# Kernel optimization log

Hardware: AMD Instinct MI355X
Metric: run time of the kernel (lower is better)

## Reference

```python
import jax, jax.numpy as jnp
import numpy as np

B, N, DX, E, H, HD, KH, FF = 8, 8192, 2, 128, 8, 16, 32, 128
G1, G2, PMAX = 32, 32, 32


def _ln(x, g, b):
    mu = jnp.mean(x, axis=-1, keepdims=True)
    var = jnp.mean((x - mu) ** 2, axis=-1, keepdims=True)
    return (x - mu) * jax.lax.rsqrt(var + 1e-5) * g + b


def _cumcount_row(idx):
    # for each element, number of earlier elements with the same value (stable)
    n = idx.shape[0]
    order = jnp.argsort(idx)  # stable
    si = idx[order]
    ar = jnp.arange(n)
    is_start = jnp.concatenate([jnp.ones((1,), bool), si[1:] != si[:-1]])
    seg_start = jax.lax.associative_scan(jnp.maximum, jnp.where(is_start, ar, 0))
    return jnp.zeros(n, jnp.int32).at[order].set((ar - seg_start).astype(jnp.int32))


def _forward(x, z, latent, Wq, Wk, Wv, Wo, bo, kW1, kb1, kW2, kb2,
             lnq_g, lnq_b, lnk_g, lnk_b, ln2_g, ln2_b, fW1, fb1, fW2, fb2,
             grid_n1, grid_n2, max_patch, num_heads):
    Bb, Nn, dx = x.shape
    e = latent.shape[0]
    dims = (grid_n1, grid_n2)
    M = grid_n1 * grid_n2
    P = max_patch
    h = num_heads
    hd = Wq.shape[1] // h
    # grid range from data (margin = 0), regular grid via linspace
    mins = [jnp.min(x[:, :, i]) for i in range(dx)]
    maxs = [jnp.max(x[:, :, i]) for i in range(dx)]
    axes = [jnp.linspace(mins[i], maxs[i], dims[i]) for i in range(dx)]
    x_grid = jnp.stack(jnp.meshgrid(*axes, indexing="ij"), axis=-1)  # [G1,G2,dx]
    x_grid_flat = x_grid.reshape(M, dx)
    # nearest grid cell per point: regular grid -> per-dim rounding
    flat = None
    for i in range(dx):
        step = (maxs[i] - mins[i]) / (dims[i] - 1)
        ii = jnp.clip(jnp.round((x[..., i] - mins[i]) / step), 0, dims[i] - 1).astype(jnp.int32)
        flat = ii if flat is None else flat * dims[i] + ii
    cell = flat  # [B,N]
    cumc = jax.vmap(_cumcount_row)(cell)          # slot within cell
    slot = jnp.where(cumc < P, cumc, P)           # overflow -> dummy slot (dropped)
    bidx = jnp.broadcast_to(jnp.arange(Bb)[:, None], (Bb, Nn))
    # scatter points into per-cell padded neighbour sets [B, M, P, d]
    jx = jnp.zeros((Bb, M, P + 1, dx), x.dtype).at[bidx, cell, slot].set(x)[:, :, :P]
    jz = jnp.zeros((Bb, M, P + 1, e), z.dtype).at[bidx, cell, slot].set(z)[:, :, :P]
    msk = jnp.zeros((Bb, M, P + 1), bool).at[bidx, cell, slot].set(True)[:, :, :P]
    xg = jnp.broadcast_to(x_grid_flat[None], (Bb, M, dx))
    zg = jnp.broadcast_to(latent[None, None, :], (Bb, M, e))
    # concatenate_x_grid=True: grid token prepended, always attended
    joint_x = jnp.concatenate([xg[:, :, None, :], jx], axis=2).reshape(Bb * M, P + 1, dx)
    joint_z = jnp.concatenate([zg[:, :, None, :], jz], axis=2).reshape(Bb * M, P + 1, e)
    att_mask = jnp.concatenate([jnp.ones((Bb, M, 1), bool), msk], axis=2).reshape(Bb * M, P + 1)
    xq = xg.reshape(Bb * M, 1, dx)
    zq = zg.reshape(Bb * M, 1, e)
    T = Bb * M
    # masked translation-equivariant cross-attention (pre-norm layer)
    q = jnp.einsum("tqe,ef->tqf", _ln(zq, lnq_g, lnq_b), Wq).reshape(T, 1, h, hd)
    zk_n = _ln(joint_z, lnk_g, lnk_b)
    k = jnp.einsum("tke,ef->tkf", zk_n, Wk).reshape(T, P + 1, h, hd)
    v = jnp.einsum("tke,ef->tkf", zk_n, Wv).reshape(T, P + 1, h, hd)
    dots = jnp.einsum("tqhd,tkhd->thqk", q, k) / jnp.sqrt(jnp.asarray(hd, q.dtype))
    diff = joint_x[:, None, :, :] - xq[:, :, None, :]            # [T,1,P+1,dx]
    kb = jnp.maximum(diff @ kW1 + kb1, 0.0) @ kW2 + kb2          # kernel bias [T,1,P+1,h]
    dots = dots + jnp.transpose(kb, (0, 3, 1, 2))
    dots = jnp.where(att_mask[:, None, None, :], dots, -1e9)
    A = jax.nn.softmax(dots, axis=-1)                            # [T,h,1,P+1]
    out = jnp.einsum("thqk,tkhd->tqhd", A, v).reshape(T, 1, h * hd)
    z_new = zq + out @ Wo + bo
    z_new = z_new + (jnp.maximum(_ln(z_new, ln2_g, ln2_b) @ fW1 + fb1, 0.0) @ fW2 + fb2)
    x_new = jnp.einsum("tqk,tkd->tqd", jnp.mean(A, axis=1), joint_x)  # TE location update
    x_grid_out = x_new.reshape(Bb, grid_n1, grid_n2, dx)
    z_grid_out = z_new.reshape(Bb, grid_n1, grid_n2, e)
    return (x_grid_out, z_grid_out)


def setup_inputs():
    key = jax.random.key(0)
    ks = jax.random.split(key, 12)
    s = 0.05
    return {
        "x": jax.random.uniform(ks[0], (B, N, DX), jnp.float32),
        "z": jax.random.normal(ks[1], (B, N, E), jnp.float32),
        "grid_n1": G1, "grid_n2": G2, "max_patch": PMAX, "num_heads": H,
        "latent": jax.random.normal(ks[2], (E,), jnp.float32),
        "Wq": jax.random.normal(ks[3], (E, H * HD), jnp.float32) * s,
        "Wk": jax.random.normal(ks[4], (E, H * HD), jnp.float32) * s,
        "Wv": jax.random.normal(ks[5], (E, H * HD), jnp.float32) * s,
        "Wo": jax.random.normal(ks[6], (H * HD, E), jnp.float32) * s,
        "bo": jnp.zeros((E,), jnp.float32),
        "kW1": jax.random.normal(ks[7], (DX, KH), jnp.float32) * s,
        "kb1": jnp.zeros((KH,), jnp.float32),
        "kW2": jax.random.normal(ks[8], (KH, H), jnp.float32) * s,
        "kb2": jnp.zeros((H,), jnp.float32),
        "lnq_g": jnp.ones((E,), jnp.float32), "lnq_b": jnp.zeros((E,), jnp.float32),
        "lnk_g": jnp.ones((E,), jnp.float32), "lnk_b": jnp.zeros((E,), jnp.float32),
        "ln2_g": jnp.ones((E,), jnp.float32), "ln2_b": jnp.zeros((E,), jnp.float32),
        "fW1": jax.random.normal(ks[9], (E, FF), jnp.float32) * s,
        "fb1": jnp.zeros((FF,), jnp.float32),
        "fW2": jax.random.normal(ks[10], (FF, E), jnp.float32) * s,
        "fb2": jnp.zeros((E,), jnp.float32),
    }


def reference(x, z, grid_n1, grid_n2, max_patch, num_heads, latent, Wq, Wk, Wv, Wo, bo,
              kW1, kb1, kW2, kb2, lnq_g, lnq_b, lnk_g, lnk_b, ln2_g, ln2_b,
              fW1, fb1, fW2, fb2):
    return _forward(x, z, latent, Wq, Wk, Wv, Wo, bo, kW1, kb1, kW2, kb2,
                    lnq_g, lnq_b, lnk_g, lnk_b, ln2_g, ln2_b, fW1, fb1, fW2, fb2,
                    grid_n1, grid_n2, max_patch, num_heads)
```

## Files before the change

### kernel.cpp

```cpp
#include <hip/hip_runtime.h>
#include <stdint.h>

#define NB 8
#define NN 8192
#define NE 128
#define NH 8
#define NHD 16
#define NKH 32
#define NFF 128
#define NG 32
#define NM 1024
#define NP 32
#define NT 8192
#define NPTS 65536

typedef __attribute__((ext_vector_type(8))) short bf16x8_t;
typedef __attribute__((ext_vector_type(4))) float f32x4_t;

#define WS_MM      0
#define WS_D0      64
#define WS_Q       128
#define WS_VG      640
#define WS_PART    1152
#define WS_CNT     2048
#define WS_CELL    34816
#define WS_PIDX    296960
#define WS_WKVT    1345536
#define WS_WOT     1411072
#define WS_FW1T    1443840
#define WS_FW2T    1476608
#define WS_OUTA    1509376
#define WS_KV      3606528

__device__ __forceinline__ unsigned short f2bf(float f) {
    unsigned u = __float_as_uint(f);
    u += 0x7FFFu + ((u >> 16) & 1u);
    return (unsigned short)(u >> 16);
}
__device__ __forceinline__ float bf2f(unsigned short h) {
    return __uint_as_float(((unsigned)h) << 16);
}
__device__ __forceinline__ float bflo(unsigned w) { return __uint_as_float(w << 16); }
__device__ __forceinline__ float bfhi(unsigned w) { return __uint_as_float(w & 0xFFFF0000u); }

__global__ __launch_bounds__(256) void k_setup(
        const float* __restrict__ x,
        const float* __restrict__ Wk, const float* __restrict__ Wv, const float* __restrict__ Wo,
        const float* __restrict__ fW1, const float* __restrict__ fW2,
        const float* __restrict__ latent, const float* __restrict__ Wq,
        const float* __restrict__ lnq_g, const float* __restrict__ lnq_b,
        const float* __restrict__ lnk_g, const float* __restrict__ lnk_b,
        const float* __restrict__ kb1, const float* __restrict__ kW2, const float* __restrict__ kb2,
        int* __restrict__ cnt,
        unsigned short* __restrict__ WkvT, unsigned short* __restrict__ WoT,
        unsigned short* __restrict__ fW1T, unsigned short* __restrict__ fW2T,
        float* __restrict__ ws_q, float* __restrict__ ws_vg, float* __restrict__ ws_d0,
        float4* __restrict__ part) {
    int blk = blockIdx.x;
    int t = threadIdx.x;
    if (blk < 20) {
        __shared__ float s_t[64][65];
        const float* src; unsigned short* dst;
        int n0, k0, srcN0;
        if (blk < 8) {
            int tn = blk >> 1, tk = blk & 1;
            n0 = tn * 64; k0 = tk * 64;
            dst = WkvT;
            if (n0 < 128) { src = Wk; srcN0 = n0; }
            else          { src = Wv; srcN0 = n0 - 128; }
        } else {
            int m = (blk - 8) >> 2, s4 = (blk - 8) & 3;
            int tn = s4 >> 1, tk = s4 & 1;
            n0 = tn * 64; k0 = tk * 64; srcN0 = n0;
            src = (m == 0) ? Wo : (m == 1) ? fW1 : fW2;
            dst = (m == 0) ? WoT : (m == 1) ? fW1T : fW2T;
        }
        int tx = t & 63, ty = t >> 6;
        #pragma unroll
        for (int r = 0; r < 16; ++r) {
            int kr = r * 4 + ty;
            s_t[kr][tx] = src[(k0 + kr) * 128 + srcN0 + tx];
        }
        __syncthreads();
        #pragma unroll
        for (int r = 0; r < 16; ++r) {
            int nr = r * 4 + ty;
            dst[(n0 + nr) * 128 + k0 + tx] = f2bf(s_t[tx][nr]);
        }
    } else if (blk < 52) {
        int idx = (blk - 20) * 256 + t;
        cnt[idx] = 0;
    } else if (blk == 52) {
        __shared__ float s_qn[128], s_kn[128], s_q[128], s_kg[128];
        __shared__ float s_mu, s_rstd;
        if (t < 64) {
            float v0 = latent[t], v1 = latent[t + 64];
            float s = v0 + v1;
            for (int m = 32; m > 0; m >>= 1) s += __shfl_xor(s, m);
            float mu = s * (1.0f / 128.0f);
            float d0 = v0 - mu, d1 = v1 - mu;
            float q = d0 * d0 + d1 * d1;
            for (int m = 32; m > 0; m >>= 1) q += __shfl_xor(q, m);
            if (t == 0) { s_mu = mu; s_rstd = rsqrtf(q * (1.0f / 128.0f) + 1e-5f); }
        }
        __syncthreads();
        if (t < 128) {
            float nv = (latent[t] - s_mu) * s_rstd;
            s_qn[t] = nv * lnq_g[t] + lnq_b[t];
            s_kn[t] = nv * lnk_g[t] + lnk_b[t];
        }
        __syncthreads();
        if (t < 128) {
            float aq = 0.f, ak = 0.f, av = 0.f;
            for (int e = 0; e < 128; ++e) {
                aq += s_qn[e] * Wq[e * 128 + t];
                ak += s_kn[e] * Wk[e * 128 + t];
                av += s_kn[e] * Wv[e * 128 + t];
            }
            s_q[t] = aq; s_kg[t] = ak;
            ws_q[t] = aq; ws_vg[t] = av;
        }
        __syncthreads();
        if (t < 8) {
            float acc = 0.f;
            for (int d = 0; d < 16; ++d) acc += s_q[t * 16 + d] * s_kg[t * 16 + d];
            float kb0 = kb2[t];
            for (int j = 0; j < 32; ++j) kb0 += fmaxf(kb1[j], 0.f) * kW2[j * 8 + t];
            ws_d0[t] = acc * 0.25f + kb0;
        }
    } else {
        __shared__ float s_red[4][4];
        int pb = blk - 53;
        const float4* xp = (const float4*)x + pb * 1024;
        float mn0 = 1e30f, mx0 = -1e30f, mn1 = 1e30f, mx1 = -1e30f;
        #pragma unroll
        for (int it = 0; it < 4; ++it) {
            float4 v = xp[it * 256 + t];
            mn0 = fminf(mn0, fminf(v.x, v.z)); mx0 = fmaxf(mx0, fmaxf(v.x, v.z));
            mn1 = fminf(mn1, fminf(v.y, v.w)); mx1 = fmaxf(mx1, fmaxf(v.y, v.w));
        }
        #pragma unroll
        for (int m = 32; m > 0; m >>= 1) {
            mn0 = fminf(mn0, __shfl_xor(mn0, m)); mx0 = fmaxf(mx0, __shfl_xor(mx0, m));
            mn1 = fminf(mn1, __shfl_xor(mn1, m)); mx1 = fmaxf(mx1, __shfl_xor(mx1, m));
        }
        int w = t >> 6;
        if ((t & 63) == 0) {
            s_red[w][0] = mn0; s_red[w][1] = mn1; s_red[w][2] = mx0; s_red[w][3] = mx1;
        }
        __syncthreads();
        if (t == 0) {
            float a0 = fminf(fminf(s_red[0][0], s_red[1][0]), fminf(s_red[2][0], s_red[3][0]));
            float a1 = fminf(fminf(s_red[0][1], s_red[1][1]), fminf(s_red[2][1], s_red[3][1]));
            float b0 = fmaxf(fmaxf(s_red[0][2], s_red[1][2]), fmaxf(s_red[2][2], s_red[3][2]));
            float b1 = fmaxf(fmaxf(s_red[0][3], s_red[1][3]), fmaxf(s_red[2][3], s_red[3][3]));
            part[pb] = make_float4(a0, a1, b0, b1);
        }
    }
}

__global__ __launch_bounds__(256) void k_bin(const float* __restrict__ x,
        const float4* __restrict__ part, float* __restrict__ mm,
        int* __restrict__ cell, int* __restrict__ cnt, int* __restrict__ ptIdx) {
    int t = threadIdx.x;
    int l = t & 63;
    float mn0 = 1e30f, mn1 = 1e30f, mx0 = -1e30f, mx1 = -1e30f;
    if (l < 32) { float4 p = part[l]; mn0 = p.x; mn1 = p.y; mx0 = p.z; mx1 = p.w; }
    #pragma unroll
    for (int m = 32; m > 0; m >>= 1) {
        mn0 = fminf(mn0, __shfl_xor(mn0, m)); mx0 = fmaxf(mx0, __shfl_xor(mx0, m));
        mn1 = fminf(mn1, __shfl_xor(mn1, m)); mx1 = fmaxf(mx1, __shfl_xor(mx1, m));
    }
    if (blockIdx.x == 0 && t == 0) {
        mm[0] = mn0; mm[1] = mn1; mm[2] = mx0; mm[3] = mx1;
    }
    int i = blockIdx.x * 256 + t;
    float st0 = (mx0 - mn0) / 31.0f, st1 = (mx1 - mn1) / 31.0f;
    float2 xv = ((const float2*)x)[i];
    int i0 = (int)rintf((xv.x - mn0) / st0); i0 = min(max(i0, 0), 31);
    int i1 = (int)rintf((xv.y - mn1) / st1); i1 = min(max(i1, 0), 31);
    int c = i0 * 32 + i1;
    cell[i] = c;
    int bb = i >> 13;
    int slot = atomicAdd(&cnt[bb * NM + c], 1);
    if (slot < NP) ptIdx[(bb * NM + c) * NP + slot] = i & (NN - 1);
}

__global__ __launch_bounds__(256) void k_kvfix(const float* __restrict__ z,
        const float* __restrict__ lnk_g, const float* __restrict__ lnk_b,
        const unsigned short* __restrict__ WkvT, unsigned short* __restrict__ kv,
        const int* __restrict__ cell, int* __restrict__ cnt, int* __restrict__ ptIdx) {
    int t = threadIdx.x;
    if (blockIdx.x >= 1024) {
        int wave = (blockIdx.x - 1024) * 4 + (t >> 6);
        int lane = t & 63;
        int wbase = wave * 16;
        int cval = (lane < 16) ? cnt[wbase + lane] : 0;
        unsigned long long ovf = __ballot(cval > NP);
        while (ovf) {
            int s = __ffsll((long long)ovf) - 1;
            ovf &= ovf - 1;
            int wid = wbase + s;
            int b = wid >> 10, mycell = wid & 1023;
            const int* cb = cell + b * NN;
            int run = 0;
            for (int ch = 0; ch < NN / 64 && run < NP; ++ch) {
                int n = ch * 64 + lane;
                bool match = (cb[n] == mycell);
                unsigned long long mask = __ballot(match);
                if (match) {
                    int rank = run + __popcll(mask & ((1ull << lane) - 1ull));
                    if (rank < NP) ptIdx[wid * NP + rank] = n;
                }
                run += __popcll(mask);
            }
            if (lane == 0) cnt[wid] = NP;
        }
        return;
    }
    __shared__ unsigned short s_zn[64][136];
    __shared__ unsigned short s_stage[4][16][68];
    int w = t >> 6, lane = t & 63;
    long base = (long)blockIdx.x * 64;
    int sub = lane >> 5;
    int lq = lane & 31;
    int mrow = lane & 15, quad = lane >> 4;

    bf16x8_t afrag[4][4];
    #pragma unroll
    for (int j = 0; j < 4; ++j) {
        int ft = w * 4 + j;
        const unsigned short* ap = WkvT + (ft * 16 + mrow) * 128 + quad * 8;
        #pragma unroll
        for (int kc = 0; kc < 4; ++kc)
            afrag[j][kc] = *(const bf16x8_t*)(ap + kc * 32);
    }

    float4 g4 = ((const float4*)lnk_g)[lq];
    float4 b4 = ((const float4*)lnk_b)[lq];
    float4 v[8];
    #pragma unroll
    for (int i = 0; i < 8; ++i) {
        int pl = w * 16 + i * 2 + sub;
        v[i] = ((const float4*)z)[(base + pl) * 32 + lq];
    }
    #pragma unroll
    for (int i = 0; i < 8; ++i) {
        int pl = w * 16 + i * 2 + sub;
        float sum = v[i].x + v[i].y + v[i].z + v[i].w;
        float ssq = v[i].x * v[i].x + v[i].y * v[i].y + v[i].z * v[i].z + v[i].w * v[i].w;
        #pragma unroll
        for (int m = 1; m < 32; m <<= 1) {
            sum += __shfl_xor(sum, m);
            ssq += __shfl_xor(ssq, m);
        }
        float mu = sum * (1.0f / 128.0f);
        float var = fmaxf(ssq * (1.0f / 128.0f) - mu * mu, 0.0f);
        float rstd = rsqrtf(var + 1e-5f);
        float n0 = (v[i].x - mu) * rstd * g4.x + b4.x;
        float n1 = (v[i].y - mu) * rstd * g4.y + b4.y;
        float n2 = (v[i].z - mu) * rstd * g4.z + b4.z;
        float n3 = (v[i].w - mu) * rstd * g4.w + b4.w;
        unsigned d0 = (unsigned)f2bf(n0) | ((unsigned)f2bf(n1) << 16);
        unsigned d1 = (unsigned)f2bf(n2) | ((unsigned)f2bf(n3) << 16);
        *(uint2*)&s_zn[pl][lq * 4] = make_uint2(d0, d1);
    }
    __syncthreads();

    #pragma unroll
    for (int tau = 0; tau < 4; ++tau) {
        bf16x8_t bfrag[4];
        #pragma unroll
        for (int kc = 0; kc < 4; ++kc)
            bfrag[kc] = *(const bf16x8_t*)&s_zn[tau * 16 + mrow][kc * 32 + quad * 8];
        #pragma unroll
        for (int j = 0; j < 4; ++j) {
            f32x4_t acc = {0.f, 0.f, 0.f, 0.f};
            #pragma unroll
            for (int kc = 0; kc < 4; ++kc)
                acc = __builtin_amdgcn_mfma_f32_16x16x32_bf16(afrag[j][kc], bfrag[kc], acc, 0, 0, 0);
            unsigned d0 = (unsigned)f2bf(acc[0]) | ((unsigned)f2bf(acc[1]) << 16);
            unsigned d1 = (unsigned)f2bf(acc[2]) | ((unsigned)f2bf(acc[3]) << 16);
            *(uint2*)&s_stage[w][mrow][j * 16 + quad * 4] = make_uint2(d0, d1);
        }
        int tok = lane >> 3, u = lane & 7;
        long tk0 = base + tau * 16;
        uint4 ra = *(const uint4*)&s_stage[w][tok][u * 8];
        *(uint4*)(kv + (tk0 + tok) * 256 + w * 64 + u * 8) = ra;
        uint4 rb = *(const uint4*)&s_stage[w][tok + 8][u * 8];
        *(uint4*)(kv + (tk0 + tok + 8) * 256 + w * 64 + u * 8) = rb;
    }
}

__global__ __launch_bounds__(256) void k_attn(const float* __restrict__ x,
        const int* __restrict__ cnt, const int* __restrict__ ptIdx,
        const float* __restrict__ mm, const unsigned short* __restrict__ kv,
        const float* __restrict__ ws_q, const float* __restrict__ ws_vg,
        const float* __restrict__ ws_d0,
        const float* __restrict__ kW1, const float* __restrict__ kb1,
        const float* __restrict__ kW2, const float* __restrict__ kb2,
        unsigned short* __restrict__ outA, float* __restrict__ xout) {
    int t = threadIdx.x;
    int l = t & 63;
    int bm = blockIdx.x * 4 + (t >> 6);
    int b = bm >> 10;
    int h = l >> 3, jp = l & 7;

    float mn0 = mm[0], mn1 = mm[1], mx0 = mm[2], mx1 = mm[3];
    int i0 = (bm & 1023) >> 5, i1 = bm & 31;
    float st0 = (mx0 - mn0) / 31.0f, st1 = (mx1 - mn1) / 31.0f;
    float xg0 = (i0 == 31) ? mx0 : mn0 + i0 * st0;
    float xg1 = (i1 == 31) ? mx1 : mn1 + i1 * st1;
    int c = min(cnt[bm], NP);

    float q0 = ws_q[2 * l] * 0.25f, q1 = ws_q[2 * l + 1] * 0.25f;
    float vg0 = ws_vg[2 * l], vg1 = ws_vg[2 * l + 1];
    float ag = ws_d0[h];
    float kb2h = kb2[h];
    float w1a[4], w1b[4], b1v[4], w2v[4];
    #pragma unroll
    for (int m = 0; m < 4; ++m) {
        int j = jp + 8 * m;
        w1a[m] = kW1[j]; w1b[m] = kW1[32 + j]; b1v[m] = kb1[j]; w2v[m] = kW2[j * 8 + h];
    }

    int idxreg = 0; float x0r = 0.f, x1r = 0.f;
    if (l < c) {
        idxreg = ptIdx[bm * NP + l];
        float2 xv = ((const float2*)x)[(size_t)b * NN + idxreg];
        x0r = xv.x; x1r = xv.y;
    }

    unsigned vreg[NP];
    float areg[4];
    #pragma unroll
    for (int k = 0; k < NP; ++k) vreg[k] = 0u;
    areg[0] = areg[1] = areg[2] = areg[3] = -1e30f;

    #pragma unroll
    for (int key = 0; key < NP; ++key) {
        if (key < c) {
            int idxk = __shfl(idxreg, key);
            const unsigned* rowp = (const unsigned*)kv + ((size_t)(b * NN + idxk) << 7);
            unsigned kw = rowp[l];
            vreg[key] = rowp[64 + l];
            float d0 = __shfl(x0r, key) - xg0;
            float d1 = __shfl(x1r, key) - xg1;
            float part = q0 * bflo(kw) + q1 * bfhi(kw);
            #pragma unroll
            for (int m = 0; m < 4; ++m) {
                float hj = fmaf(d0, w1a[m], fmaf(d1, w1b[m], b1v[m]));
                hj = fmaxf(hj, 0.f);
                part = fmaf(hj, w2v[m], part);
            }
            part += __shfl_xor(part, 1);
            part += __shfl_xor(part, 2);
            part += __shfl_xor(part, 4);
            float score = part + kb2h;
            if (jp == (key & 7)) areg[key >> 3] = score;
        }
    }

    float mx = fmaxf(fmaxf(areg[0], areg[1]), fmaxf(areg[2], areg[3]));
    mx = fmaxf(mx, ag);
    mx = fmaxf(mx, __shfl_xor(mx, 1));
    mx = fmaxf(mx, __shfl_xor(mx, 2));
    mx = fmaxf(mx, __shfl_xor(mx, 4));
    float e0 = __expf(areg[0] - mx), e1 = __expf(areg[1] - mx);
    float e2 = __expf(areg[2] - mx), e3 = __expf(areg[3] - mx);
    float eg = __expf(ag - mx);
    float s = e0 + e1 + e2 + e3;
    s += __shfl_xor(s, 1);
    s += __shfl_xor(s, 2);
    s += __shfl_xor(s, 4);
    s += eg;
    float inv = 1.0f / s;

    float accA = eg * inv * vg0, accB = eg * inv * vg1;
    #pragma unroll
    for (int key = 0; key < NP; ++key) {
        if (key < c) {
            int src = (l & 56) | (key & 7);
            float em = (key >> 3) == 0 ? e0 : (key >> 3) == 1 ? e1 : (key >> 3) == 2 ? e2 : e3;
            float a = __shfl(em, src) * inv;
            unsigned vw = vreg[key];
            accA = fmaf(a, bflo(vw), accA);
            accB = fmaf(a, bfhi(vw), accB);
        }
    }
    unsigned ow = ((unsigned)f2bf(accB) << 16) | (unsigned)f2bf(accA);
    ((unsigned*)outA)[(size_t)bm * 64 + l] = ow;

    float s0 = e0 * inv, s1 = e1 * inv, s2 = e2 * inv, s3 = e3 * inv, sg = eg * inv;
    #pragma unroll
    for (int m = 8; m <= 32; m <<= 1) {
        s0 += __shfl_xor(s0, m); s1 += __shfl_xor(s1, m);
        s2 += __shfl_xor(s2, m); s3 += __shfl_xor(s3, m);
        sg += __shfl_xor(sg, m);
    }
    float px0 = 0.f, px1 = 0.f;
    {
        float xx0, xx1;
        xx0 = __shfl(x0r, jp);      xx1 = __shfl(x1r, jp);
        px0 = fmaf(s0, xx0, px0);   px1 = fmaf(s0, xx1, px1);
        xx0 = __shfl(x0r, jp + 8);  xx1 = __shfl(x1r, jp + 8);
        px0 = fmaf(s1, xx0, px0);   px1 = fmaf(s1, xx1, px1);
        xx0 = __shfl(x0r, jp + 16); xx1 = __shfl(x1r, jp + 16);
        px0 = fmaf(s2, xx0, px0);   px1 = fmaf(s2, xx1, px1);
        xx0 = __shfl(x0r, jp + 24); xx1 = __shfl(x1r, jp + 24);
        px0 = fmaf(s3, xx0, px0);   px1 = fmaf(s3, xx1, px1);
    }
    px0 += __shfl_xor(px0, 1); px1 += __shfl_xor(px1, 1);
    px0 += __shfl_xor(px0, 2); px1 += __shfl_xor(px1, 2);
    px0 += __shfl_xor(px0, 4); px1 += __shfl_xor(px1, 4);
    if (l == 0) {
        xout[bm * 2]     = (px0 + sg * xg0) * 0.125f;
        xout[bm * 2 + 1] = (px1 + sg * xg1) * 0.125f;
    }
}

__global__ __launch_bounds__(256) void k_ffn(const unsigned short* __restrict__ outA,
        const float* __restrict__ latent, const float* __restrict__ bo,
        const float* __restrict__ ln2_g, const float* __restrict__ ln2_b,
        const float* __restrict__ fb1, const float* __restrict__ fb2,
        const unsigned short* __restrict__ WoT, const unsigned short* __restrict__ fW1T,
        const unsigned short* __restrict__ fW2T, float* __restrict__ zout) {
    __shared__ unsigned short s_a[32][136];
    __shared__ unsigned short s_a2[32][136];
    __shared__ float s_z[32][128];
    __shared__ float s_lat[128], s_g2[128], s_b2[128], s_fb1v[128], s_fb2v[128];
    int t = threadIdx.x;
    long base = (long)blockIdx.x * 32;
    if (t < 128) {
        s_lat[t] = latent[t] + bo[t];
        s_g2[t] = ln2_g[t]; s_b2[t] = ln2_b[t];
        s_fb1v[t] = fb1[t]; s_fb2v[t] = fb2[t];
    }
    {
        const uint4* src4 = (const uint4*)((const uint32_t*)outA + base * 64);
        for (int i = t; i < 512; i += 256) {
            int row = i >> 4, off = (i & 15) * 8;
            *(uint4*)&s_a[row][off] = src4[i];
        }
    }
    __syncthreads();
    int w = t >> 6, lane = t & 63;
    int mrow = lane & 15, quad = lane >> 4;
    int rt = w >> 1;
    int ct0 = (w & 1) * 4;
    {
        bf16x8_t a[4];
        for (int kc = 0; kc < 4; ++kc)
            a[kc] = *(const bf16x8_t*)&s_a[rt * 16 + mrow][kc * 32 + quad * 8];
        for (int cc = 0; cc < 4; ++cc) {
            int ct = ct0 + cc;
            f32x4_t acc = {0.f, 0.f, 0.f, 0.f};
            const unsigned short* bp = WoT + (ct * 16 + mrow) * 128 + quad * 8;
            for (int kc = 0; kc < 4; ++kc)
                acc = __builtin_amdgcn_mfma_f32_16x16x32_bf16(a[kc], *(const bf16x8_t*)(bp + kc * 32), acc, 0, 0, 0);
            for (int r = 0; r < 4; ++r) {
                int row = rt * 16 + quad * 4 + r, f = ct * 16 + mrow;
                s_z[row][f] = acc[r] + s_lat[f];
            }
        }
    }
    __syncthreads();
    for (int i = 0; i < 8; ++i) {
        int row = w * 8 + i;
        float v0 = s_z[row][lane], v1 = s_z[row][lane + 64];
        float s = v0 + v1;
        for (int m = 32; m > 0; m >>= 1) s += __shfl_xor(s, m);
        float mu = s * (1.0f / 128.0f);
        float d0 = v0 - mu, d1 = v1 - mu;
        float q = d0 * d0 + d1 * d1;
        for (int m = 32; m > 0; m >>= 1) q += __shfl_xor(q, m);
        float rstd = rsqrtf(q * (1.0f / 128.0f) + 1e-5f);
        s_a2[row][lane]      = f2bf(d0 * rstd * s_g2[lane] + s_b2[lane]);
        s_a2[row][lane + 64] = f2bf(d1 * rstd * s_g2[lane + 64] + s_b2[lane + 64]);
    }
    __syncthreads();
    {
        bf16x8_t a[4];
        for (int kc = 0; kc < 4; ++kc)
            a[kc] = *(const bf16x8_t*)&s_a2[rt * 16 + mrow][kc * 32 + quad * 8];
        for (int cc = 0; cc < 4; ++cc) {
            int ct = ct0 + cc;
            f32x4_t acc = {0.f, 0.f, 0.f, 0.f};
            const unsigned short* bp = fW1T + (ct * 16 + mrow) * 128 + quad * 8;
            for (int kc = 0; kc < 4; ++kc)
                acc = __builtin_amdgcn_mfma_f32_16x16x32_bf16(a[kc], *(const bf16x8_t*)(bp + kc * 32), acc, 0, 0, 0);
            for (int r = 0; r < 4; ++r) {
                int row = rt * 16 + quad * 4 + r, f = ct * 16 + mrow;
                s_a[row][f] = f2bf(fmaxf(acc[r] + s_fb1v[f], 0.f));
            }
        }
    }
    __syncthreads();
    {
        bf16x8_t a[4];
        for (int kc = 0; kc < 4; ++kc)
            a[kc] = *(const bf16x8_t*)&s_a[rt * 16 + mrow][kc * 32 + quad * 8];
        for (int cc = 0; cc < 4; ++cc) {
            int ct = ct0 + cc;
            f32x4_t acc = {0.f, 0.f, 0.f, 0.f};
            const unsigned short* bp = fW2T + (ct * 16 + mrow) * 128 + quad * 8;
            for (int kc = 0; kc < 4; ++kc)
                acc = __builtin_amdgcn_mfma_f32_16x16x32_bf16(a[kc], *(const bf16x8_t*)(bp + kc * 32), acc, 0, 0, 0);
            for (int r = 0; r < 4; ++r) {
                int row = rt * 16 + quad * 4 + r, f = ct * 16 + mrow;
                zout[(base + row) * 128 + f] = s_z[row][f] + acc[r] + s_fb2v[f];
            }
        }
    }
}

extern "C" void kernel_launch(void* const* d_in, const int* in_sizes, int n_in,
                              void* d_out, int out_size, void* d_ws, size_t ws_size,
                              hipStream_t stream) {
    const float* x     = (const float*)d_in[0];
    const float* z     = (const float*)d_in[1];
    const float* latent= (const float*)d_in[6];
    const float* Wq    = (const float*)d_in[7];
    const float* Wk    = (const float*)d_in[8];
    const float* Wv    = (const float*)d_in[9];
    const float* Wo    = (const float*)d_in[10];
    const float* bo    = (const float*)d_in[11];
    const float* kW1   = (const float*)d_in[12];
    const float* kb1   = (const float*)d_in[13];
    const float* kW2   = (const float*)d_in[14];
    const float* kb2   = (const float*)d_in[15];
    const float* lnq_g = (const float*)d_in[16];
    const float* lnq_b = (const float*)d_in[17];
    const float* lnk_g = (const float*)d_in[18];
    const float* lnk_b = (const float*)d_in[19];
    const float* ln2_g = (const float*)d_in[20];
    const float* ln2_b = (const float*)d_in[21];
    const float* fW1   = (const float*)d_in[22];
    const float* fb1   = (const float*)d_in[23];
    const float* fW2   = (const float*)d_in[24];
    const float* fb2   = (const float*)d_in[25];

    uint8_t* ws = (uint8_t*)d_ws;
    float* mm     = (float*)(ws + WS_MM);
    float* ws_d0  = (float*)(ws + WS_D0);
    float* ws_q   = (float*)(ws + WS_Q);
    float* ws_vg  = (float*)(ws + WS_VG);
    float4* part  = (float4*)(ws + WS_PART);
    int* cnt      = (int*)(ws + WS_CNT);
    int* cell     = (int*)(ws + WS_CELL);
    int* ptIdx    = (int*)(ws + WS_PIDX);
    unsigned short* WkvT = (unsigned short*)(ws + WS_WKVT);
    unsigned short* WoT  = (unsigned short*)(ws + WS_WOT);
    unsigned short* fW1T = (unsigned short*)(ws + WS_FW1T);
    unsigned short* fW2T = (unsigned short*)(ws + WS_FW2T);
    unsigned short* outA = (unsigned short*)(ws + WS_OUTA);
    unsigned short* kv   = (unsigned short*)(ws + WS_KV);

    float* xout = (float*)d_out;
    float* zout = (float*)d_out + 16384;

    k_setup <<<85,   256, 0, stream>>>(x, Wk, Wv, Wo, fW1, fW2, latent, Wq,
                                       lnq_g, lnq_b, lnk_g, lnk_b, kb1, kW2, kb2,
                                       cnt, WkvT, WoT, fW1T, fW2T, ws_q, ws_vg, ws_d0, part);
    k_bin   <<<256,  256, 0, stream>>>(x, part, mm, cell, cnt, ptIdx);
    k_kvfix <<<1152, 256, 0, stream>>>(z, lnk_g, lnk_b, WkvT, kv, cell, cnt, ptIdx);
    k_attn  <<<2048, 256, 0, stream>>>(x, cnt, ptIdx, mm, kv, ws_q, ws_vg, ws_d0,
                                       kW1, kb1, kW2, kb2, outA, xout);
    k_ffn   <<<256,  256, 0, stream>>>(outA, latent, bo, ln2_g, ln2_b, fb1, fb2,
                                       WoT, fW1T, fW2T, zout);
}
```

Measured before the change: 181.2 us.

## Fuse binning with KV projection and FFN into attention kernel

Merges the binning kernel into the KV-projection kernel as extra blocks, moves the overflow-cell fixup into the attention kernel per wave, and fuses the Wo/LN/FFN epilogue into the attention kernel using shared memory instead of a global outA buffer. This cuts two kernel launches and a global round-trip of the attention output. In exchange, the FFN MFMAs now run on 16-row tiles with only 4 valid rows, which wastes matrix throughput. The attention kernel also gains shared memory and extra syncs that may lower occupancy.

```diff
diff --git a/kernel.cpp b/kernel.cpp
--- a/kernel.cpp
+++ b/kernel.cpp
@@ -29,7 +29,6 @@
 #define WS_WOT     1411072
 #define WS_FW1T    1443840
 #define WS_FW2T    1476608
-#define WS_OUTA    1509376
 #define WS_KV      3606528
 
 __device__ __forceinline__ unsigned short f2bf(float f) {
@@ -159,63 +158,35 @@
     }
 }
 
-__global__ __launch_bounds__(256) void k_bin(const float* __restrict__ x,
+__global__ __launch_bounds__(256) void k_binkv(
+        const float* __restrict__ x, const float* __restrict__ z,
         const float4* __restrict__ part, float* __restrict__ mm,
+        const float* __restrict__ lnk_g, const float* __restrict__ lnk_b,
+        const unsigned short* __restrict__ WkvT, unsigned short* __restrict__ kv,
         int* __restrict__ cell, int* __restrict__ cnt, int* __restrict__ ptIdx) {
     int t = threadIdx.x;
-    int l = t & 63;
-    float mn0 = 1e30f, mn1 = 1e30f, mx0 = -1e30f, mx1 = -1e30f;
-    if (l < 32) { float4 p = part[l]; mn0 = p.x; mn1 = p.y; mx0 = p.z; mx1 = p.w; }
-    #pragma unroll
-    for (int m = 32; m > 0; m >>= 1) {
-        mn0 = fminf(mn0, __shfl_xor(mn0, m)); mx0 = fmaxf(mx0, __shfl_xor(mx0, m));
-        mn1 = fminf(mn1, __shfl_xor(mn1, m)); mx1 = fmaxf(mx1, __shfl_xor(mx1, m));
-    }
-    if (blockIdx.x == 0 && t == 0) {
-        mm[0] = mn0; mm[1] = mn1; mm[2] = mx0; mm[3] = mx1;
-    }
-    int i = blockIdx.x * 256 + t;
-    float st0 = (mx0 - mn0) / 31.0f, st1 = (mx1 - mn1) / 31.0f;
-    float2 xv = ((const float2*)x)[i];
-    int i0 = (int)rintf((xv.x - mn0) / st0); i0 = min(max(i0, 0), 31);
-    int i1 = (int)rintf((xv.y - mn1) / st1); i1 = min(max(i1, 0), 31);
-    int c = i0 * 32 + i1;
-    cell[i] = c;
-    int bb = i >> 13;
-    int slot = atomicAdd(&cnt[bb * NM + c], 1);
-    if (slot < NP) ptIdx[(bb * NM + c) * NP + slot] = i & (NN - 1);
-}
-
-__global__ __launch_bounds__(256) void k_kvfix(const float* __restrict__ z,
-        const float* __restrict__ lnk_g, const float* __restrict__ lnk_b,
-        const unsigned short* __restrict__ WkvT, unsigned short* __restrict__ kv,
-        const int* __restrict__ cell, int* __restrict__ cnt, int* __restrict__ ptIdx) {
-    int t = threadIdx.x;
     if (blockIdx.x >= 1024) {
-        int wave = (blockIdx.x - 1024) * 4 + (t >> 6);
-        int lane = t & 63;
-        int wbase = wave * 16;
-        int cval = (lane < 16) ? cnt[wbase + lane] : 0;
-        unsigned long long ovf = __ballot(cval > NP);
-        while (ovf) {
-            int s = __ffsll((long long)ovf) - 1;
-            ovf &= ovf - 1;
-            int wid = wbase + s;
-            int b = wid >> 10, mycell = wid & 1023;
-            const int* cb = cell + b * NN;
-            int run = 0;
-            for (int ch = 0; ch < NN / 64 && run < NP; ++ch) {
-                int n = ch * 64 + lane;
-                bool match = (cb[n] == mycell);
-                unsigned long long mask = __ballot(match);
-                if (match) {
-                    int rank = run + __popcll(mask & ((1ull << lane) - 1ull));
-                    if (rank < NP) ptIdx[wid * NP + rank] = n;
-                }
-                run += __popcll(mask);
-            }
-            if (lane == 0) cnt[wid] = NP;
-        }
+        int l = t & 63;
+        float mn0 = 1e30f, mn1 = 1e30f, mx0 = -1e30f, mx1 = -1e30f;
+        if (l < 32) { float4 p = part[l]; mn0 = p.x; mn1 = p.y; mx0 = p.z; mx1 = p.w; }
+        #pragma unroll
+        for (int m = 32; m > 0; m >>= 1) {
+            mn0 = fminf(mn0, __shfl_xor(mn0, m)); mx0 = fmaxf(mx0, __shfl_xor(mx0, m));
+            mn1 = fminf(mn1, __shfl_xor(mn1, m)); mx1 = fmaxf(mx1, __shfl_xor(mx1, m));
+        }
+        if (blockIdx.x == 1024 && t == 0) {
+            mm[0] = mn0; mm[1] = mn1; mm[2] = mx0; mm[3] = mx1;
+        }
+        int i = (blockIdx.x - 1024) * 256 + t;
+        float st0 = (mx0 - mn0) / 31.0f, st1 = (mx1 - mn1) / 31.0f;
+        float2 xv = ((const float2*)x)[i];
+        int i0 = (int)rintf((xv.x - mn0) / st0); i0 = min(max(i0, 0), 31);
+        int i1 = (int)rintf((xv.y - mn1) / st1); i1 = min(max(i1, 0), 31);
+        int c = i0 * 32 + i1;
+        cell[i] = c;
+        int bb = i >> 13;
+        int slot = atomicAdd(&cnt[bb * NM + c], 1);
+        if (slot < NP) ptIdx[(bb * NM + c) * NP + slot] = i & (NN - 1);
         return;
     }
     __shared__ unsigned short s_zn[64][136];
@@ -293,16 +264,31 @@
 }
 
 __global__ __launch_bounds__(256) void k_attn(const float* __restrict__ x,
-        const int* __restrict__ cnt, const int* __restrict__ ptIdx,
+        const int* __restrict__ cell, const int* __restrict__ cnt, int* __restrict__ ptIdx,
         const float* __restrict__ mm, const unsigned short* __restrict__ kv,
         const float* __restrict__ ws_q, const float* __restrict__ ws_vg,
         const float* __restrict__ ws_d0,
         const float* __restrict__ kW1, const float* __restrict__ kb1,
         const float* __restrict__ kW2, const float* __restrict__ kb2,
-        unsigned short* __restrict__ outA, float* __restrict__ xout) {
+        const float* __restrict__ latent, const float* __restrict__ bo,
+        const float* __restrict__ ln2_g, const float* __restrict__ ln2_b,
+        const float* __restrict__ fb1, const float* __restrict__ fb2,
+        const unsigned short* __restrict__ WoT, const unsigned short* __restrict__ fW1T,
+        const unsigned short* __restrict__ fW2T,
+        float* __restrict__ xout, float* __restrict__ zout) {
+    __shared__ unsigned short s_a[16][136];
+    __shared__ unsigned short s_a2[16][136];
+    __shared__ float s_z[4][128];
+    __shared__ float s_lat[128], s_g2[128], s_b2[128], s_fb1v[128], s_fb2v[128];
     int t = threadIdx.x;
     int l = t & 63;
-    int bm = blockIdx.x * 4 + (t >> 6);
+    int w = t >> 6;
+    if (t < 128) {
+        s_lat[t] = latent[t] + bo[t];
+        s_g2[t] = ln2_g[t]; s_b2[t] = ln2_b[t];
+        s_fb1v[t] = fb1[t]; s_fb2v[t] = fb2[t];
+    }
+    int bm = blockIdx.x * 4 + w;
     int b = bm >> 10;
     int h = l >> 3, jp = l & 7;
 
@@ -311,7 +297,23 @@
     float st0 = (mx0 - mn0) / 31.0f, st1 = (mx1 - mn1) / 31.0f;
     float xg0 = (i0 == 31) ? mx0 : mn0 + i0 * st0;
     float xg1 = (i1 == 31) ? mx1 : mn1 + i1 * st1;
-    int c = min(cnt[bm], NP);
+    int craw = cnt[bm];
+    int c = min(craw, NP);
+    if (craw > NP) {
+        int mycell = bm & 1023;
+        const int* cb = cell + b * NN;
+        int run = 0;
+        for (int ch = 0; ch < NN / 64 && run < NP; ++ch) {
+            int n = ch * 64 + l;
+            bool match = (cb[n] == mycell);
+            unsigned long long mask = __ballot(match);
+            if (match) {
+                int rank = run + __popcll(mask & ((1ull << l) - 1ull));
+                if (rank < NP) ptIdx[bm * NP + rank] = n;
+            }
+            run += __popcll(mask);
+        }
+    }
 
     float q0 = ws_q[2 * l] * 0.25f, q1 = ws_q[2 * l + 1] * 0.25f;
     float vg0 = ws_vg[2 * l], vg1 = ws_vg[2 * l + 1];
@@ -389,7 +391,7 @@
         }
     }
     unsigned ow = ((unsigned)f2bf(accB) << 16) | (unsigned)f2bf(accA);
-    ((unsigned*)outA)[(size_t)bm * 64 + l] = ow;
+    *(unsigned*)&s_a[w][2 * l] = ow;
 
     float s0 = e0 * inv, s1 = e1 * inv, s2 = e2 * inv, s3 = e3 * inv, sg = eg * inv;
     #pragma unroll
@@ -417,98 +419,86 @@
         xout[bm * 2]     = (px0 + sg * xg0) * 0.125f;
         xout[bm * 2 + 1] = (px1 + sg * xg1) * 0.125f;
     }
-}
-
-__global__ __launch_bounds__(256) void k_ffn(const unsigned short* __restrict__ outA,
-        const float* __restrict__ latent, const float* __restrict__ bo,
-        const float* __restrict__ ln2_g, const float* __restrict__ ln2_b,
-        const float* __restrict__ fb1, const float* __restrict__ fb2,
-        const unsigned short* __restrict__ WoT, const unsigned short* __restrict__ fW1T,
-        const unsigned short* __restrict__ fW2T, float* __restrict__ zout) {
-    __shared__ unsigned short s_a[32][136];
-    __shared__ unsigned short s_a2[32][136];
-    __shared__ float s_z[32][128];
-    __shared__ float s_lat[128], s_g2[128], s_b2[128], s_fb1v[128], s_fb2v[128];
-    int t = threadIdx.x;
-    long base = (long)blockIdx.x * 32;
-    if (t < 128) {
-        s_lat[t] = latent[t] + bo[t];
-        s_g2[t] = ln2_g[t]; s_b2[t] = ln2_b[t];
-        s_fb1v[t] = fb1[t]; s_fb2v[t] = fb2[t];
-    }
-    {
-        const uint4* src4 = (const uint4*)((const uint32_t*)outA + base * 64);
-        for (int i = t; i < 512; i += 256) {
-            int row = i >> 4, off = (i & 15) * 8;
-            *(uint4*)&s_a[row][off] = src4[i];
-        }
-    }
+
     __syncthreads();
-    int w = t >> 6, lane = t & 63;
-    int mrow = lane & 15, quad = lane >> 4;
-    int rt = w >> 1;
-    int ct0 = (w & 1) * 4;
+    int mrow = l & 15, quad = l >> 4;
+    int base4 = blockIdx.x * 4;
     {
         bf16x8_t a[4];
+        #pragma unroll
         for (int kc = 0; kc < 4; ++kc)
-            a[kc] = *(const bf16x8_t*)&s_a[rt * 16 + mrow][kc * 32 + quad * 8];
-        for (int cc = 0; cc < 4; ++cc) {
-            int ct = ct0 + cc;
+            a[kc] = *(const bf16x8_t*)&s_a[mrow][kc * 32 + quad * 8];
+        #pragma unroll
+        for (int cc = 0; cc < 2; ++cc) {
+            int ct = w * 2 + cc;
             f32x4_t acc = {0.f, 0.f, 0.f, 0.f};
             const unsigned short* bp = WoT + (ct * 16 + mrow) * 128 + quad * 8;
+            #pragma unroll
             for (int kc = 0; kc < 4; ++kc)
                 acc = __builtin_amdgcn_mfma_f32_16x16x32_bf16(a[kc], *(const bf16x8_t*)(bp + kc * 32), acc, 0, 0, 0);
-            for (int r = 0; r < 4; ++r) {
-                int row = rt * 16 + quad * 4 + r, f = ct * 16 + mrow;
-                s_z[row][f] = acc[r] + s_lat[f];
+            if (quad == 0) {
+                int f = ct * 16 + mrow;
+                #pragma unroll
+                for (int r = 0; r < 4; ++r) s_z[r][f] = acc[r] + s_lat[f];
             }
         }
     }
     __syncthreads();
-    for (int i = 0; i < 8; ++i) {
-        int row = w * 8 + i;
-        float v0 = s_z[row][lane], v1 = s_z[row][lane + 64];
-        float s = v0 + v1;
-        for (int m = 32; m > 0; m >>= 1) s += __shfl_xor(s, m);
-        float mu = s * (1.0f / 128.0f);
+    {
+        float v0 = s_z[w][l], v1 = s_z[w][l + 64];
+        float ssum = v0 + v1;
+        #pragma unroll
+        for (int m = 32; m > 0; m >>= 1) ssum += __shfl_xor(ssum, m);
+        float mu = ssum * (1.0f / 128.0f);
         float d0 = v0 - mu, d1 = v1 - mu;
-        float q = d0 * d0 + d1 * d1;
-        for (int m = 32; m > 0; m >>= 1) q += __shfl_xor(q, m);
-        float rstd = rsqrtf(q * (1.0f / 128.0f) + 1e-5f);
-        s_a2[row][lane]      = f2bf(d0 * rstd * s_g2[lane] + s_b2[lane]);
-        s_a2[row][lane + 64] = f2bf(d1 * rstd * s_g2[lane + 64] + s_b2[lane + 64]);
+        float qq = d0 * d0 + d1 * d1;
+        #pragma unroll
+        for (int m = 32; m > 0; m >>= 1) qq += __shfl_xor(qq, m);
+        float rstd = rsqrtf(qq * (1.0f / 128.0f) + 1e-5f);
+        s_a2[w][l]      = f2bf(d0 * rstd * s_g2[l] + s_b2[l]);
+        s_a2[w][l + 64] = f2bf(d1 * rstd * s_g2[l + 64] + s_b2[l + 64]);
     }
     __syncthreads();
     {
         bf16x8_t a[4];
+        #pragma unroll
         for (int kc = 0; kc < 4; ++kc)
-            a[kc] = *(const bf16x8_t*)&s_a2[rt * 16 + mrow][kc * 32 + quad * 8];
-        for (int cc = 0; cc < 4; ++cc) {
-            int ct = ct0 + cc;
+            a[kc] = *(const bf16x8_t*)&s_a2[mrow][kc * 32 + quad * 8];
+        #pragma unroll
+        for (int cc = 0; cc < 2; ++cc) {
+            int ct = w * 2 + cc;
             f32x4_t acc = {0.f, 0.f, 0.f, 0.f};
             const unsigned short* bp = fW1T + (ct * 16 + mrow) * 128 + quad * 8;
+            #pragma unroll
             for (int kc = 0; kc < 4; ++kc)
                 acc = __builtin_amdgcn_mfma_f32_16x16x32_bf16(a[kc], *(const bf16x8_t*)(bp + kc * 32), acc, 0, 0, 0);
-            for (int r = 0; r < 4; ++r) {
-                int row = rt * 16 + quad * 4 + r, f = ct * 16 + mrow;
-                s_a[row][f] = f2bf(fmaxf(acc[r] + s_fb1v[f], 0.f));
+            if (quad == 0) {
+                int f = ct * 16 + mrow;
+                #pragma unroll
+                for (int r = 0; r < 4; ++r)
+                    s_a[r][f] = f2bf(fmaxf(acc[r] + s_fb1v[f], 0.f));
             }
         }
     }
     __syncthreads();
     {
         bf16x8_t a[4];
+        #pragma unroll
         for (int kc = 0; kc < 4; ++kc)
-            a[kc] = *(const bf16x8_t*)&s_a[rt * 16 + mrow][kc * 32 + quad * 8];
-        for (int cc = 0; cc < 4; ++cc) {
-            int ct = ct0 + cc;
+            a[kc] = *(const bf16x8_t*)&s_a[mrow][kc * 32 + quad * 8];
+        #pragma unroll
+        for (int cc = 0; cc < 2; ++cc) {
+            int ct = w * 2 + cc;
             f32x4_t acc = {0.f, 0.f, 0.f, 0.f};
             const unsigned short* bp = fW2T + (ct * 16 + mrow) * 128 + quad * 8;
+            #pragma unroll
             for (int kc = 0; kc < 4; ++kc)
                 acc = __builtin_amdgcn_mfma_f32_16x16x32_bf16(a[kc], *(const bf16x8_t*)(bp + kc * 32), acc, 0, 0, 0);
-            for (int r = 0; r < 4; ++r) {
-                int row = rt * 16 + quad * 4 + r, f = ct * 16 + mrow;
-                zout[(base + row) * 128 + f] = s_z[row][f] + acc[r] + s_fb2v[f];
+            if (quad == 0) {
+                int f = ct * 16 + mrow;
+                #pragma unroll
+                for (int r = 0; r < 4; ++r)
+                    zout[(base4 + r) * 128 + f] = s_z[r][f] + acc[r] + s_fb2v[f];
             }
         }
     }
@@ -553,7 +543,6 @@
     unsigned short* WoT  = (unsigned short*)(ws + WS_WOT);
     unsigned short* fW1T = (unsigned short*)(ws + WS_FW1T);
     unsigned short* fW2T = (unsigned short*)(ws + WS_FW2T);
-    unsigned short* outA = (unsigned short*)(ws + WS_OUTA);
     unsigned short* kv   = (unsigned short*)(ws + WS_KV);
 
     float* xout = (float*)d_out;
@@ -562,10 +551,10 @@
     k_setup <<<85,   256, 0, stream>>>(x, Wk, Wv, Wo, fW1, fW2, latent, Wq,
                                        lnq_g, lnq_b, lnk_g, lnk_b, kb1, kW2, kb2,
                                        cnt, WkvT, WoT, fW1T, fW2T, ws_q, ws_vg, ws_d0, part);
-    k_bin   <<<256,  256, 0, stream>>>(x, part, mm, cell, cnt, ptIdx);
-    k_kvfix <<<1152, 256, 0, stream>>>(z, lnk_g, lnk_b, WkvT, kv, cell, cnt, ptIdx);
-    k_attn  <<<2048, 256, 0, stream>>>(x, cnt, ptIdx, mm, kv, ws_q, ws_vg, ws_d0,
-                                       kW1, kb1, kW2, kb2, outA, xout);
-    k_ffn   <<<256,  256, 0, stream>>>(outA, latent, bo, ln2_g, ln2_b, fb1, fb2,
-                                       WoT, fW1T, fW2T, zout);
+    k_binkv <<<1280, 256, 0, stream>>>(x, z, part, mm, lnk_g, lnk_b, WkvT, kv,
+                                       cell, cnt, ptIdx);
+    k_attn  <<<2048, 256, 0, stream>>>(x, cell, cnt, ptIdx, mm, kv, ws_q, ws_vg, ws_d0,
+                                       kW1, kb1, kW2, kb2,
+                                       latent, bo, ln2_g, ln2_b, fb1, fb2,
+                                       WoT, fW1T, fW2T, xout, zout);
 }
```

Result: slower. 187.4 us (+3.5%).
